# Optimization experiments

Hardware: AMD Instinct MI355X
Metric: run time of the kernel (lower is better)

Reference implementation:

```python
import jax, jax.numpy as jnp
import numpy as np

N_NODES = 50000
N_EDGES = 800000
IN_DIM = 256
HID = 32
HEADS = 8
OUT_DIM = 16


def gat_layer(x, src, dst, W, att_s, att_d, bias, concat):
    """PyG-style GATConv (eval mode, add_self_loops already applied to src/dst)."""
    N = x.shape[0]
    H, C = att_s.shape
    h = (x @ W).reshape(N, H, C)                       # [N, H, C]
    a_s = jnp.sum(h * att_s, axis=-1)                  # [N, H]
    a_d = jnp.sum(h * att_d, axis=-1)                  # [N, H]
    alpha = jax.nn.leaky_relu(a_s[src] + a_d[dst], negative_slope=0.2)  # [E, H]
    # segment softmax over edges grouped by destination node
    m = jax.ops.segment_max(alpha, dst, num_segments=N)                 # [N, H]
    e = jnp.exp(alpha - m[dst])
    s = jax.ops.segment_sum(e, dst, num_segments=N)
    coef = e / (s[dst] + 1e-16)                                         # [E, H]
    out = jax.ops.segment_sum(coef[:, :, None] * h[src], dst, num_segments=N)  # [N, H, C]
    out = out.reshape(N, H * C) if concat else out.mean(axis=1)
    return out + bias


def setup_inputs() -> dict:
    key = jax.random.key(0)
    ks = jax.random.split(key, 10)
    x = jax.random.normal(ks[0], (N_NODES, IN_DIM), dtype=jnp.float32)
    edge_index = jax.random.randint(ks[1], (2, N_EDGES), 0, N_NODES, dtype=jnp.int32)
    sc = 0.05
    W1 = jax.random.normal(ks[2], (IN_DIM, HEADS * HID), dtype=jnp.float32) * sc
    att_src1 = jax.random.normal(ks[3], (HEADS, HID), dtype=jnp.float32) * sc
    att_dst1 = jax.random.normal(ks[4], (HEADS, HID), dtype=jnp.float32) * sc
    b1 = jnp.zeros((HEADS * HID,), dtype=jnp.float32)
    W2 = jax.random.normal(ks[5], (HEADS * HID, OUT_DIM), dtype=jnp.float32) * sc
    att_src2 = jax.random.normal(ks[6], (1, OUT_DIM), dtype=jnp.float32) * sc
    att_dst2 = jax.random.normal(ks[7], (1, OUT_DIM), dtype=jnp.float32) * sc
    b2 = jnp.zeros((OUT_DIM,), dtype=jnp.float32)
    return {"x": x, "edge_index": edge_index,
            "W1": W1, "att_src1": att_src1, "att_dst1": att_dst1, "b1": b1,
            "W2": W2, "att_src2": att_src2, "att_dst2": att_dst2, "b2": b2}


def reference(x, edge_index, W1, att_src1, att_dst1, b1, W2, att_src2, att_dst2, b2):
    N = x.shape[0]
    loops = jnp.arange(N, dtype=edge_index.dtype)      # GATConv add_self_loops=True
    src = jnp.concatenate([edge_index[0], loops])
    dst = jnp.concatenate([edge_index[1], loops])
    h = jax.nn.elu(gat_layer(x, src, dst, W1, att_src1, att_dst1, b1, concat=True))
    out = gat_layer(h, src, dst, W2, att_src2, att_dst2, b2, concat=False)
    return out
```

## Files before the change

### kernel.cpp

```cpp
#include <hip/hip_runtime.h>

#define N_NODES 50000
#define N_EDGES 800000
#define E_TOT   (N_EDGES + N_NODES)
#define IN_DIM  256
#define HID     32
#define HEADS   8
#define D1      256
#define OUT_DIM 16

#define SCAN_NB ((N_NODES + 255) / 256)
#define CNT8_NB ((N_EDGES + 2047) / 2048)
#define G1_NB   ((D1 / 128) * ((N_NODES + 127) / 128))

typedef __attribute__((ext_vector_type(8))) short bf16x8;
typedef __attribute__((ext_vector_type(4))) float f32x4;
typedef __attribute__((ext_vector_type(4))) _Float16 half4;
typedef __attribute__((ext_vector_type(8))) _Float16 half8;

__device__ __forceinline__ unsigned short f2bf(float f) {
  unsigned u = __float_as_uint(f);
  return (unsigned short)((u + 0x7FFFu + ((u >> 16) & 1u)) >> 16);
}
__device__ __forceinline__ float bf2f(unsigned short b) {
  return __uint_as_float(((unsigned)b) << 16);
}
__device__ __forceinline__ float lrelu(float a) { return (a > 0.f) ? a : 0.2f * a; }

__global__ void prep_w(const float* __restrict__ W, unsigned short* __restrict__ Wth,
                       unsigned short* __restrict__ Wtl) {
  int t = blockIdx.x * blockDim.x + threadIdx.x;
  if (t >= IN_DIM * D1) return;
  int n = t >> 8, k = t & 255;
  float v = W[k * D1 + n];
  unsigned short h = f2bf(v);
  Wth[n * IN_DIM + k] = h;
  Wtl[n * IN_DIM + k] = f2bf(v - bf2f(h));
}

__global__ __launch_bounds__(256) void gemm1_count(
    const float* __restrict__ x,
    const unsigned short* __restrict__ Bth_g, const unsigned short* __restrict__ Btl_g,
    const float* __restrict__ att_s, const float* __restrict__ att_d,
    _Float16* __restrict__ C, float* __restrict__ as_, float* __restrict__ ad_,
    const int* __restrict__ edst, int* __restrict__ deg4, int* __restrict__ rank) {
  const int bid = blockIdx.x;
  if (bid < CNT8_NB) {
    const int eb = bid * 2048 + threadIdx.x;
    #pragma unroll
    for (int u = 0; u < 8; u++) {
      int e = eb + u * 256;
      if (e < N_EDGES) {
        int d = edst[e];
        rank[e] = atomicAdd(&deg4[(d << 2) + (e & 3)], 1);
      }
    }
    return;
  }
  __shared__ short Ah[128][40], Al[128][40];
  __shared__ short Bh[128][40], Bl[128][40];
  const int gb = bid - CNT8_NB;
  const int bm = (gb >> 1) * 128, bn = (gb & 1) * 128;
  const int tid = threadIdx.x;
  const int wave = tid >> 6, lane = tid & 63;
  const int l15 = lane & 15, l4 = lane >> 4;
  f32x4 acc[8][2] = {};
  const int sr2 = tid >> 1, sc2 = (tid & 1) * 16;
  const bf16x8 zv = {0, 0, 0, 0, 0, 0, 0, 0};
  for (int k0 = 0; k0 < IN_DIM; k0 += 32) {
    int grow = bm + sr2;
    if (grow < N_NODES) {
      const float4* xp = (const float4*)&x[(size_t)grow * IN_DIM + k0 + sc2];
      #pragma unroll
      for (int j = 0; j < 4; j++) {
        float4 v = xp[j];
        ushort4 hh, ll;
        hh.x = f2bf(v.x); ll.x = f2bf(v.x - bf2f(hh.x));
        hh.y = f2bf(v.y); ll.y = f2bf(v.y - bf2f(hh.y));
        hh.z = f2bf(v.z); ll.z = f2bf(v.z - bf2f(hh.z));
        hh.w = f2bf(v.w); ll.w = f2bf(v.w - bf2f(hh.w));
        *(ushort4*)&Ah[sr2][sc2 + j * 4] = hh;
        *(ushort4*)&Al[sr2][sc2 + j * 4] = ll;
      }
    } else {
      *(bf16x8*)&Ah[sr2][sc2] = zv;
      *(bf16x8*)&Ah[sr2][sc2 + 8] = zv;
      *(bf16x8*)&Al[sr2][sc2] = zv;
      *(bf16x8*)&Al[sr2][sc2 + 8] = zv;
    }
    {
      const bf16x8* sH = (const bf16x8*)&Bth_g[(size_t)(bn + sr2) * IN_DIM + k0 + sc2];
      const bf16x8* sL = (const bf16x8*)&Btl_g[(size_t)(bn + sr2) * IN_DIM + k0 + sc2];
      *(bf16x8*)&Bh[sr2][sc2] = sH[0];
      *(bf16x8*)&Bh[sr2][sc2 + 8] = sH[1];
      *(bf16x8*)&Bl[sr2][sc2] = sL[0];
      *(bf16x8*)&Bl[sr2][sc2 + 8] = sL[1];
    }
    __syncthreads();
    bf16x8 bh0 = *(bf16x8*)&Bh[wave * 32 + l15][l4 * 8];
    bf16x8 bl0 = *(bf16x8*)&Bl[wave * 32 + l15][l4 * 8];
    bf16x8 bh1 = *(bf16x8*)&Bh[wave * 32 + 16 + l15][l4 * 8];
    bf16x8 bl1 = *(bf16x8*)&Bl[wave * 32 + 16 + l15][l4 * 8];
    #pragma unroll
    for (int i = 0; i < 8; i++) {
      bf16x8 ah = *(bf16x8*)&Ah[i * 16 + l15][l4 * 8];
      bf16x8 al = *(bf16x8*)&Al[i * 16 + l15][l4 * 8];
      acc[i][0] = __builtin_amdgcn_mfma_f32_16x16x32_bf16(ah, bh0, acc[i][0], 0, 0, 0);
      acc[i][0] = __builtin_amdgcn_mfma_f32_16x16x32_bf16(ah, bl0, acc[i][0], 0, 0, 0);
      acc[i][0] = __builtin_amdgcn_mfma_f32_16x16x32_bf16(al, bh0, acc[i][0], 0, 0, 0);
      acc[i][1] = __builtin_amdgcn_mfma_f32_16x16x32_bf16(ah, bh1, acc[i][1], 0, 0, 0);
      acc[i][1] = __builtin_amdgcn_mfma_f32_16x16x32_bf16(ah, bl1, acc[i][1], 0, 0, 0);
      acc[i][1] = __builtin_amdgcn_mfma_f32_16x16x32_bf16(al, bh1, acc[i][1], 0, 0, 0);
    }
    __syncthreads();
  }
  const int head = (bn >> 5) + wave;
  const float sA0 = att_s[head * HID + l15];
  const float sA1 = att_s[head * HID + 16 + l15];
  const float dA0 = att_d[head * HID + l15];
  const float dA1 = att_d[head * HID + 16 + l15];
  #pragma unroll
  for (int i = 0; i < 8; i++) {
    #pragma unroll
    for (int cf = 0; cf < 2; cf++) {
      const int ccol = bn + wave * 32 + cf * 16 + l15;
      #pragma unroll
      for (int r = 0; r < 4; r++) {
        int crow = bm + i * 16 + l4 * 4 + r;
        if (crow < N_NODES) C[(size_t)crow * D1 + ccol] = (_Float16)acc[i][cf][r];
      }
    }
    float ps[4], pd[4];
    #pragma unroll
    for (int r = 0; r < 4; r++) {
      ps[r] = acc[i][0][r] * sA0 + acc[i][1][r] * sA1;
      pd[r] = acc[i][0][r] * dA0 + acc[i][1][r] * dA1;
    }
    #pragma unroll
    for (int m = 1; m < 16; m <<= 1) {
      #pragma unroll
      for (int r = 0; r < 4; r++) {
        ps[r] += __shfl_xor(ps[r], m);
        pd[r] += __shfl_xor(pd[r], m);
      }
    }
    if (l15 == 0) {
      #pragma unroll
      for (int r = 0; r < 4; r++) {
        int crow = bm + i * 16 + l4 * 4 + r;
        if (crow < N_NODES) {
          as_[crow * HEADS + head] = ps[r];
          ad_[crow * HEADS + head] = pd[r];
        }
      }
    }
  }
}

__global__ __launch_bounds__(256) void scan_partial(const int* __restrict__ deg4,
                                                    int4* __restrict__ pre4,
                                                    int* __restrict__ deg,
                                                    int* __restrict__ offs,
                                                    int* __restrict__ part) {
  __shared__ int ts[256];
  const int tid = threadIdx.x;
  const int n = blockIdx.x * 256 + tid;
  int4 v = {0, 0, 0, 0};
  if (n < N_NODES) v = *(const int4*)(deg4 + n * 4);
  int4 p;
  p.x = 0; p.y = v.x; p.z = v.x + v.y; p.w = v.x + v.y + v.z;
  const int tot = p.w + v.w + 1;
  if (n < N_NODES) { pre4[n] = p; deg[n] = tot; }
  ts[tid] = (n < N_NODES) ? tot : 0;
  __syncthreads();
  for (int st = 1; st < 256; st <<= 1) {
    int t = (tid >= st) ? ts[tid - st] : 0;
    __syncthreads();
    ts[tid] += t;
    __syncthreads();
  }
  if (tid == 255) part[blockIdx.x] = ts[255];
  if (n < N_NODES) offs[n] = ts[tid] - tot;
}

__global__ __launch_bounds__(256) void scan_apply(int* __restrict__ offs,
                                                  const int* __restrict__ part,
                                                  const int* __restrict__ deg,
                                                  int* __restrict__ srcs) {
  __shared__ int sp[SCAN_NB];
  const int tid = threadIdx.x;
  if (tid < SCAN_NB) sp[tid] = part[tid];
  __syncthreads();
  if (tid == 0) {
    int run = 0;
    #pragma unroll 1
    for (int b = 0; b < SCAN_NB; b++) { int v = sp[b]; sp[b] = run; run += v; }
  }
  __syncthreads();
  int n = blockIdx.x * 256 + tid;
  if (n < N_NODES) {
    int o = offs[n] + sp[n >> 8];
    offs[n] = o;
    srcs[o + deg[n] - 1] = n;
  }
}

__global__ void scatter_edges(const int* __restrict__ esrc, const int* __restrict__ edst,
                              const int* __restrict__ offs, const int4* __restrict__ pre4,
                              const int* __restrict__ rank, int* __restrict__ srcs) {
  int e = blockIdx.x * blockDim.x + threadIdx.x;
  if (e >= N_EDGES) return;
  int s = esrc[e], d = edst[e];
  int4 p = pre4[d];
  int j = e & 3;
  int pj = (j == 0) ? p.x : (j == 1) ? p.y : (j == 2) ? p.z : p.w;
  srcs[offs[d] + pj + rank[e]] = s;
}

__global__ __launch_bounds__(256) void node_aggr1(
    const int* __restrict__ offs, const int* __restrict__ deg,
    const int* __restrict__ srcs,
    const float* __restrict__ as_, const float* __restrict__ ad_,
    const _Float16* __restrict__ h, const float* __restrict__ bias,
    _Float16* __restrict__ out) {
  const int n = blockIdx.x * 4 + (threadIdx.x >> 6);
  const int lane = threadIdx.x & 63;
  const int base = offs[n], dg = deg[n];
  const int hd = lane >> 3;
  const float adn = ad_[n * HEADS + hd];
  const unsigned c0 = lane * 4;
  float4 acc = {0.f, 0.f, 0.f, 0.f};
  float se = 0.f;
  int e = 0;
  for (; e + 8 <= dg; e += 8) {
    int s[8];
    #pragma unroll
    for (int u = 0; u < 8; u++) s[u] = __builtin_amdgcn_readfirstlane(srcs[base + e + u]);
    half4 hv[8];
    #pragma unroll
    for (int u = 0; u < 8; u++) hv[u] = *(const half4*)(h + ((unsigned)s[u] * D1 + c0));
    float ex[8];
    #pragma unroll
    for (int u = 0; u < 8; u++) ex[u] = __expf(lrelu(as_[(unsigned)s[u] * HEADS + hd] + adn));
    #pragma unroll
    for (int u = 0; u < 8; u++) {
      se += ex[u];
      acc.x += ex[u] * (float)hv[u].x; acc.y += ex[u] * (float)hv[u].y;
      acc.z += ex[u] * (float)hv[u].z; acc.w += ex[u] * (float)hv[u].w;
    }
  }
  for (; e + 4 <= dg; e += 4) {
    int s[4];
    #pragma unroll
    for (int u = 0; u < 4; u++) s[u] = __builtin_amdgcn_readfirstlane(srcs[base + e + u]);
    half4 hv[4];
    #pragma unroll
    for (int u = 0; u < 4; u++) hv[u] = *(const half4*)(h + ((unsigned)s[u] * D1 + c0));
    float ex[4];
    #pragma unroll
    for (int u = 0; u < 4; u++) ex[u] = __expf(lrelu(as_[(unsigned)s[u] * HEADS + hd] + adn));
    #pragma unroll
    for (int u = 0; u < 4; u++) {
      se += ex[u];
      acc.x += ex[u] * (float)hv[u].x; acc.y += ex[u] * (float)hv[u].y;
      acc.z += ex[u] * (float)hv[u].z; acc.w += ex[u] * (float)hv[u].w;
    }
  }
  for (; e < dg; e++) {
    int s = __builtin_amdgcn_readfirstlane(srcs[base + e]);
    float ex = __expf(lrelu(as_[(unsigned)s * HEADS + hd] + adn));
    half4 hv = *(const half4*)(h + ((unsigned)s * D1 + c0));
    se += ex;
    acc.x += ex * (float)hv.x; acc.y += ex * (float)hv.y;
    acc.z += ex * (float)hv.z; acc.w += ex * (float)hv.w;
  }
  const float inv = 1.f / (se + 1e-16f);
  float4 bv = *(const float4*)(bias + c0);
  float4 v;
  v.x = acc.x * inv + bv.x; v.y = acc.y * inv + bv.y;
  v.z = acc.z * inv + bv.z; v.w = acc.w * inv + bv.w;
  v.x = (v.x > 0.f) ? v.x : expm1f(v.x);
  v.y = (v.y > 0.f) ? v.y : expm1f(v.y);
  v.z = (v.z > 0.f) ? v.z : expm1f(v.z);
  v.w = (v.w > 0.f) ? v.w : expm1f(v.w);
  half4 ov;
  ov.x = (_Float16)v.x; ov.y = (_Float16)v.y; ov.z = (_Float16)v.z; ov.w = (_Float16)v.w;
  *(half4*)(out + ((unsigned)n * D1 + c0)) = ov;
}

__global__ __launch_bounds__(256) void gemm2_attn2(
    const _Float16* __restrict__ A, const float* __restrict__ B,
    const float* __restrict__ att_s, const float* __restrict__ att_d,
    _Float16* __restrict__ C, float* __restrict__ as_, float* __restrict__ ad_) {
  __shared__ float Bs[D1 * OUT_DIM];
  const int tid = threadIdx.x;
  #pragma unroll
  for (int i = 0; i < D1 * OUT_DIM / 4 / 256; i++)
    ((float4*)Bs)[tid + i * 256] = ((const float4*)B)[tid + i * 256];
  __syncthreads();
  const int t = blockIdx.x * 256 + tid;
  const int n = t >> 4, c = t & 15;
  const _Float16* arow = A + (size_t)n * D1;
  float acc = 0.f;
  #pragma unroll
  for (int k0 = 0; k0 < D1; k0 += 8) {
    half8 av = *(const half8*)&arow[k0];
    #pragma unroll
    for (int j = 0; j < 8; j++) acc += (float)av[j] * Bs[(k0 + j) * OUT_DIM + c];
  }
  C[t] = (_Float16)acc;
  float ps = acc * att_s[c], pd = acc * att_d[c];
  #pragma unroll
  for (int mS = 1; mS < 16; mS <<= 1) {
    ps += __shfl_xor(ps, mS);
    pd += __shfl_xor(pd, mS);
  }
  if (c == 0) { as_[n] = ps; ad_[n] = pd; }
}

__global__ __launch_bounds__(256) void node_aggr2(
    const int* __restrict__ offs, const int* __restrict__ deg,
    const int* __restrict__ srcs,
    const float* __restrict__ as_, const float* __restrict__ ad_,
    const _Float16* __restrict__ g, const float* __restrict__ bias,
    float* __restrict__ out) {
  const int n = blockIdx.x * 4 + (threadIdx.x >> 6);
  const int lane = threadIdx.x & 63;
  const int base = offs[n], dg = deg[n];
  const float adn = ad_[n];
  const int c = lane & 15, grp = lane >> 4;
  float acc = 0.f, se = 0.f;
  int e = grp;
  for (; e + 8 <= dg + grp; e += 8) {
    unsigned s0 = srcs[base + e], s1 = srcs[base + e + 4];
    float e0 = __expf(lrelu(as_[s0] + adn));
    float e1 = __expf(lrelu(as_[s1] + adn));
    float g0 = (float)g[s0 * OUT_DIM + c], g1 = (float)g[s1 * OUT_DIM + c];
    se += e0 + e1;
    acc += e0 * g0 + e1 * g1;
  }
  for (; e < dg; e += 4) {
    unsigned s = srcs[base + e];
    float ex = __expf(lrelu(as_[s] + adn));
    se += ex;
    acc += ex * (float)g[s * OUT_DIM + c];
  }
  acc += __shfl_xor(acc, 16); se += __shfl_xor(se, 16);
  acc += __shfl_xor(acc, 32); se += __shfl_xor(se, 32);
  if (lane < OUT_DIM) out[n * OUT_DIM + c] = acc / (se + 1e-16f) + bias[c];
}

extern "C" void kernel_launch(void* const* d_in, const int* in_sizes, int n_in,
                              void* d_out, int out_size, void* d_ws, size_t ws_size,
                              hipStream_t stream) {
  const float* x      = (const float*)d_in[0];
  const int*   ei     = (const int*)d_in[1];
  const float* W1     = (const float*)d_in[2];
  const float* att_s1 = (const float*)d_in[3];
  const float* att_d1 = (const float*)d_in[4];
  const float* b1     = (const float*)d_in[5];
  const float* W2     = (const float*)d_in[6];
  const float* att_s2 = (const float*)d_in[7];
  const float* att_d2 = (const float*)d_in[8];
  const float* b2     = (const float*)d_in[9];
  float* out = (float*)d_out;
  const int* esrc = ei;
  const int* edst = ei + N_EDGES;

  char* w = (char*)d_ws;
  _Float16* h1f = (_Float16*)w; w += (size_t)N_NODES * D1 * 2;
  _Float16* h2  = (_Float16*)w; w += (size_t)N_NODES * D1 * 2;
  unsigned short* W1t_hi = (unsigned short*)w;  w += (size_t)IN_DIM * D1 * 2;
  unsigned short* W1t_lo = (unsigned short*)w;  w += (size_t)IN_DIM * D1 * 2;
  float* as1 = (float*)w;       w += (size_t)N_NODES * HEADS * 4;
  float* ad1 = (float*)w;       w += (size_t)N_NODES * HEADS * 4;
  _Float16* g2 = (_Float16*)w;  w += (size_t)N_NODES * OUT_DIM * 2;
  float* as2 = (float*)w;       w += (size_t)N_NODES * 4;
  float* ad2 = (float*)w;       w += (size_t)N_NODES * 4;
  int* deg4  = (int*)w;         w += (size_t)N_NODES * 16;
  int4* pre4 = (int4*)w;        w += (size_t)N_NODES * 16;
  int* deg   = (int*)w;         w += (size_t)N_NODES * 4;
  int* offs  = (int*)w;         w += (size_t)N_NODES * 4;
  int* part  = (int*)w;         w += (size_t)256 * 4;
  int* rank  = (int*)w;         w += (size_t)N_EDGES * 4;
  int* srcs  = (int*)w;         w += (size_t)E_TOT * 4;

  hipMemsetAsync(deg4, 0, (size_t)N_NODES * 16, stream);

  prep_w<<<IN_DIM * D1 / 256, 256, 0, stream>>>(W1, W1t_hi, W1t_lo);

  gemm1_count<<<CNT8_NB + G1_NB, 256, 0, stream>>>(
      x, W1t_hi, W1t_lo, att_s1, att_d1, h1f, as1, ad1, edst, deg4, rank);

  scan_partial<<<SCAN_NB, 256, 0, stream>>>(deg4, pre4, deg, offs, part);
  scan_apply<<<SCAN_NB, 256, 0, stream>>>(offs, part, deg, srcs);
  scatter_edges<<<(N_EDGES + 255) / 256, 256, 0, stream>>>(esrc, edst, offs, pre4, rank, srcs);

  node_aggr1<<<N_NODES / 4, 256, 0, stream>>>(offs, deg, srcs, as1, ad1, h1f, b1, h2);

  gemm2_attn2<<<N_NODES * OUT_DIM / 256, 256, 0, stream>>>(
      h2, W2, att_s2, att_d2, g2, as2, ad2);

  node_aggr2<<<N_NODES / 4, 256, 0, stream>>>(offs, deg, srcs, as2, ad2, g2, b2, out);
}
```

Baseline: 209.1 us.

## Fuse layer-2 projection and attention logits into layer-1 aggregation kernel

The second-layer GEMM and attention-score computation now run in the epilogue of the first aggregation kernel. Each wavefront projects its ELU output row through W2 (held transposed in shared memory) and reduces across lanes with shuffles. This removes the fp16 hidden-feature buffer write and re-read and one kernel launch. Separately, per-node offsets plus per-bucket prefixes are precomputed into offs4 so the edge scatter does one gather instead of two. The cost is a 16-value, 6-step shuffle reduction per node, and each block must stage 16 KB of W2 into shared memory.

Measured after the change: 245.5 us. +17.4%, slower.

```diff
diff --git a/kernel.cpp b/kernel.cpp
--- a/kernel.cpp
+++ b/kernel.cpp
@@ -186,6 +186,8 @@
 __global__ __launch_bounds__(256) void scan_apply(int* __restrict__ offs,
                                                   const int* __restrict__ part,
                                                   const int* __restrict__ deg,
+                                                  const int4* __restrict__ pre4,
+                                                  int4* __restrict__ offs4,
                                                   int* __restrict__ srcs) {
   __shared__ int sp[SCAN_NB];
   const int tid = threadIdx.x;
@@ -201,30 +203,44 @@
   if (n < N_NODES) {
     int o = offs[n] + sp[n >> 8];
     offs[n] = o;
+    int4 p = pre4[n];
+    int4 o4;
+    o4.x = o + p.x; o4.y = o + p.y; o4.z = o + p.z; o4.w = o + p.w;
+    offs4[n] = o4;
     srcs[o + deg[n] - 1] = n;
   }
 }
 
 __global__ void scatter_edges(const int* __restrict__ esrc, const int* __restrict__ edst,
-                              const int* __restrict__ offs, const int4* __restrict__ pre4,
-                              const int* __restrict__ rank, int* __restrict__ srcs) {
+                              const int* __restrict__ offs4, const int* __restrict__ rank,
+                              int* __restrict__ srcs) {
   int e = blockIdx.x * blockDim.x + threadIdx.x;
   if (e >= N_EDGES) return;
   int s = esrc[e], d = edst[e];
-  int4 p = pre4[d];
-  int j = e & 3;
-  int pj = (j == 0) ? p.x : (j == 1) ? p.y : (j == 2) ? p.z : p.w;
-  srcs[offs[d] + pj + rank[e]] = s;
-}
-
-__global__ __launch_bounds__(256) void node_aggr1(
+  srcs[offs4[(d << 2) + (e & 3)] + rank[e]] = s;
+}
+
+__global__ __launch_bounds__(256) void node_aggr1_g2(
     const int* __restrict__ offs, const int* __restrict__ deg,
     const int* __restrict__ srcs,
     const float* __restrict__ as_, const float* __restrict__ ad_,
     const _Float16* __restrict__ h, const float* __restrict__ bias,
-    _Float16* __restrict__ out) {
-  const int n = blockIdx.x * 4 + (threadIdx.x >> 6);
-  const int lane = threadIdx.x & 63;
+    const float* __restrict__ W2, const float* __restrict__ att_s2,
+    const float* __restrict__ att_d2,
+    _Float16* __restrict__ g2, float* __restrict__ as2, float* __restrict__ ad2) {
+  __shared__ float Bst[OUT_DIM * D1];
+  __shared__ float s2v[OUT_DIM], d2v[OUT_DIM];
+  const int tid = threadIdx.x;
+  #pragma unroll
+  for (int i = 0; i < OUT_DIM * D1 / 256; i++) {
+    int idx = tid + i * 256;
+    Bst[(idx & 15) * D1 + (idx >> 4)] = W2[idx];
+  }
+  if (tid < OUT_DIM) { s2v[tid] = att_s2[tid]; d2v[tid] = att_d2[tid]; }
+  __syncthreads();
+
+  const int n = blockIdx.x * 4 + (tid >> 6);
+  const int lane = tid & 63;
   const int base = offs[n], dg = deg[n];
   const int hd = lane >> 3;
   const float adn = ad_[n * HEADS + hd];
@@ -283,39 +299,32 @@
   v.y = (v.y > 0.f) ? v.y : expm1f(v.y);
   v.z = (v.z > 0.f) ? v.z : expm1f(v.z);
   v.w = (v.w > 0.f) ? v.w : expm1f(v.w);
-  half4 ov;
-  ov.x = (_Float16)v.x; ov.y = (_Float16)v.y; ov.z = (_Float16)v.z; ov.w = (_Float16)v.w;
-  *(half4*)(out + ((unsigned)n * D1 + c0)) = ov;
-}
-
-__global__ __launch_bounds__(256) void gemm2_attn2(
-    const _Float16* __restrict__ A, const float* __restrict__ B,
-    const float* __restrict__ att_s, const float* __restrict__ att_d,
-    _Float16* __restrict__ C, float* __restrict__ as_, float* __restrict__ ad_) {
-  __shared__ float Bs[D1 * OUT_DIM];
-  const int tid = threadIdx.x;
+
+  float p[OUT_DIM];
   #pragma unroll
-  for (int i = 0; i < D1 * OUT_DIM / 4 / 256; i++)
-    ((float4*)Bs)[tid + i * 256] = ((const float4*)B)[tid + i * 256];
-  __syncthreads();
-  const int t = blockIdx.x * 256 + tid;
-  const int n = t >> 4, c = t & 15;
-  const _Float16* arow = A + (size_t)n * D1;
-  float acc = 0.f;
+  for (int c = 0; c < OUT_DIM; c++) {
+    float4 wv = *(const float4*)&Bst[c * D1 + c0];
+    p[c] = v.x * wv.x + v.y * wv.y + v.z * wv.z + v.w * wv.w;
+  }
   #pragma unroll
-  for (int k0 = 0; k0 < D1; k0 += 8) {
-    half8 av = *(const half8*)&arow[k0];
-    #pragma unroll
-    for (int j = 0; j < 8; j++) acc += (float)av[j] * Bs[(k0 + j) * OUT_DIM + c];
-  }
-  C[t] = (_Float16)acc;
-  float ps = acc * att_s[c], pd = acc * att_d[c];
-  #pragma unroll
-  for (int mS = 1; mS < 16; mS <<= 1) {
-    ps += __shfl_xor(ps, mS);
-    pd += __shfl_xor(pd, mS);
-  }
-  if (c == 0) { as_[n] = ps; ad_[n] = pd; }
+  for (int m = 1; m < 64; m <<= 1) {
+    #pragma unroll
+    for (int c = 0; c < OUT_DIM; c++) p[c] += __shfl_xor(p[c], m);
+  }
+  if (lane == 0) {
+    _Float16 gh[OUT_DIM];
+    float ps = 0.f, pd = 0.f;
+    #pragma unroll
+    for (int c = 0; c < OUT_DIM; c++) {
+      gh[c] = (_Float16)p[c];
+      ps += p[c] * s2v[c];
+      pd += p[c] * d2v[c];
+    }
+    *(half8*)(g2 + n * OUT_DIM) = *(half8*)gh;
+    *(half8*)(g2 + n * OUT_DIM + 8) = *(half8*)(gh + 8);
+    as2[n] = ps;
+    ad2[n] = pd;
+  }
 }
 
 __global__ __launch_bounds__(256) void node_aggr2(
@@ -369,7 +378,6 @@
 
   char* w = (char*)d_ws;
   _Float16* h1f = (_Float16*)w; w += (size_t)N_NODES * D1 * 2;
-  _Float16* h2  = (_Float16*)w; w += (size_t)N_NODES * D1 * 2;
   unsigned short* W1t_hi = (unsigned short*)w;  w += (size_t)IN_DIM * D1 * 2;
   unsigned short* W1t_lo = (unsigned short*)w;  w += (size_t)IN_DIM * D1 * 2;
   float* as1 = (float*)w;       w += (size_t)N_NODES * HEADS * 4;
@@ -379,6 +387,7 @@
   float* ad2 = (float*)w;       w += (size_t)N_NODES * 4;
   int* deg4  = (int*)w;         w += (size_t)N_NODES * 16;
   int4* pre4 = (int4*)w;        w += (size_t)N_NODES * 16;
+  int4* offs4 = (int4*)w;       w += (size_t)N_NODES * 16;
   int* deg   = (int*)w;         w += (size_t)N_NODES * 4;
   int* offs  = (int*)w;         w += (size_t)N_NODES * 4;
   int* part  = (int*)w;         w += (size_t)256 * 4;
@@ -393,13 +402,11 @@
       x, W1t_hi, W1t_lo, att_s1, att_d1, h1f, as1, ad1, edst, deg4, rank);
 
   scan_partial<<<SCAN_NB, 256, 0, stream>>>(deg4, pre4, deg, offs, part);
-  scan_apply<<<SCAN_NB, 256, 0, stream>>>(offs, part, deg, srcs);
-  scatter_edges<<<(N_EDGES + 255) / 256, 256, 0, stream>>>(esrc, edst, offs, pre4, rank, srcs);
-
-  node_aggr1<<<N_NODES / 4, 256, 0, stream>>>(offs, deg, srcs, as1, ad1, h1f, b1, h2);
-
-  gemm2_attn2<<<N_NODES * OUT_DIM / 256, 256, 0, stream>>>(
-      h2, W2, att_s2, att_d2, g2, as2, ad2);
+  scan_apply<<<SCAN_NB, 256, 0, stream>>>(offs, part, deg, pre4, offs4, srcs);
+  scatter_edges<<<(N_EDGES + 255) / 256, 256, 0, stream>>>(esrc, edst, (const int*)offs4, rank, srcs);
+
+  node_aggr1_g2<<<N_NODES / 4, 256, 0, stream>>>(
+      offs, deg, srcs, as1, ad1, h1f, b1, W2, att_s2, att_d2, g2, as2, ad2);
 
   node_aggr2<<<N_NODES / 4, 256, 0, stream>>>(offs, deg, srcs, as2, ad2, g2, b2, out);
 }
```
